# Kernel optimization log

Measured on AMD Instinct MI355X. Metric: run time of the kernel, lower is better.

## Reference

```python
import jax, jax.numpy as jnp
import numpy as np

D_MODEL = 2048
NUM_HEADS = 32
NUM_KV_HEADS = 8
D_K = D_MODEL // NUM_HEADS
B, S = 2, 2048


def setup_inputs() -> dict:
    key = jax.random.key(0)
    ks = jax.random.split(key, 6)
    sc = 1.0 / np.sqrt(D_MODEL)
    x = jax.random.normal(ks[0], (B, S, D_MODEL), dtype=jnp.float32)
    mask = jnp.tril(jnp.ones((S, S), dtype=jnp.float32))[None, None]  # [1,1,S,S]
    return {
        'x': x,
        'mask': mask,
        'Wq': jax.random.normal(ks[1], (D_MODEL, D_MODEL), jnp.float32) * sc,
        'bq': jnp.zeros((D_MODEL,), jnp.float32),
        'Wk': jax.random.normal(ks[2], (D_MODEL, NUM_KV_HEADS * D_K), jnp.float32) * sc,
        'bk': jnp.zeros((NUM_KV_HEADS * D_K,), jnp.float32),
        'Wv': jax.random.normal(ks[3], (D_MODEL, NUM_KV_HEADS * D_K), jnp.float32) * sc,
        'bv': jnp.zeros((NUM_KV_HEADS * D_K,), jnp.float32),
        'Wo': jax.random.normal(ks[4], (D_MODEL, D_MODEL), jnp.float32) * sc,
        'bo': jnp.zeros((D_MODEL,), jnp.float32),
    }


def reference(x, mask, Wq, bq, Wk, bk, Wv, bv, Wo, bo):
    b, s, _ = x.shape
    g = NUM_HEADS // NUM_KV_HEADS  # queries per kv head
    Q = (x @ Wq + bq).reshape(b, s, NUM_HEADS, D_K).transpose(0, 2, 1, 3)      # [b,h,s,dk]
    K = (x @ Wk + bk).reshape(b, s, NUM_KV_HEADS, D_K).transpose(0, 2, 1, 3)   # [b,kv,s,dk]
    V = (x @ Wv + bv).reshape(b, s, NUM_KV_HEADS, D_K).transpose(0, 2, 1, 3)
    # group queries per kv head instead of repeat_interleave on K/V
    Qg = Q.reshape(b, NUM_KV_HEADS, g, s, D_K)
    scores = jnp.einsum('bkgqd,bkld->bkgql', Qg, K) / np.sqrt(D_K)             # [b,kv,g,s,s]
    scores = jnp.where(mask[:, :, None] == 0, -1e9, scores)
    attn = jax.nn.softmax(scores, axis=-1)
    out = jnp.einsum('bkgql,bkld->bkgqd', attn, V)                              # [b,kv,g,s,dk]
    out = out.reshape(b, NUM_HEADS, s, D_K).transpose(0, 2, 1, 3).reshape(b, s, D_MODEL)
    return out @ Wo + bo
```

## Files before the change

### kernel.cpp

```cpp
#include <hip/hip_runtime.h>
#include <stdint.h>

typedef __bf16 bf16x8 __attribute__((ext_vector_type(8)));
typedef float  f32x4  __attribute__((ext_vector_type(4)));

__device__ __forceinline__ f32x4 mfma16(bf16x8 a, bf16x8 b, f32x4 c) {
    return __builtin_amdgcn_mfma_f32_16x16x32_bf16(a, b, c, 0, 0, 0);
}

__device__ __forceinline__ uint16_t f2bf(float f) {
    union { __bf16 b; uint16_t u; } cv; cv.b = (__bf16)f; return cv.u;
}

typedef __attribute__((address_space(3))) void as3_void;
typedef __attribute__((address_space(1))) void as1_void;
__device__ __forceinline__ void async_ld16(const void* g, void* l) {
    __builtin_amdgcn_global_load_lds((const as1_void*)g, (as3_void*)l, 16, 0, 0);
}


__global__ void convert_f32_bf16(const float* __restrict__ in, uint16_t* __restrict__ out, int n) {
    int i = (blockIdx.x * 256 + threadIdx.x) * 4;
    if (i >= n) return;
    float4 v = *(const float4*)(in + i);
    ushort4 o;
    o.x = f2bf(v.x); o.y = f2bf(v.y); o.z = f2bf(v.z); o.w = f2bf(v.w);
    *(ushort4*)(out + i) = o;
}

__global__ void transpose_f32_bf16(const float* __restrict__ in, uint16_t* __restrict__ out,
                                   int ldin, int out_off, int ldout) {
    __shared__ float tile[32][33];
    const int c0 = blockIdx.x << 5, r0 = blockIdx.y << 5;
    const int tx = threadIdx.x, ty = threadIdx.y;
#pragma unroll
    for (int i = 0; i < 4; ++i)
        tile[ty + i * 8][tx] = in[(size_t)(r0 + ty + i * 8) * ldin + c0 + tx];
    __syncthreads();
#pragma unroll
    for (int i = 0; i < 4; ++i)
        out[(size_t)(out_off + c0 + ty + i * 8) * ldout + r0 + tx] = f2bf(tile[tx][ty + i * 8]);
}

__global__ void transpose_v(const uint16_t* __restrict__ qkv, uint16_t* __restrict__ vt) {
    __shared__ uint16_t tile[32][33];
    const int c0 = blockIdx.x << 5, r0 = blockIdx.y << 5, b = blockIdx.z;
    const int tx = threadIdx.x, ty = threadIdx.y;
#pragma unroll
    for (int i = 0; i < 4; ++i)
        tile[ty + i * 8][tx] = qkv[(size_t)(b * 2048 + r0 + ty + i * 8) * 3072 + 2560 + c0 + tx];
    __syncthreads();
#pragma unroll
    for (int i = 0; i < 4; ++i)
        vt[(size_t)(b * 512 + c0 + ty + i * 8) * 2048 + r0 + tx] = tile[tx][ty + i * 8];
}

__global__ void concat_bias(const float* __restrict__ bq, const float* __restrict__ bk,
                            const float* __restrict__ bv, float* __restrict__ out) {
    int i = blockIdx.x * 256 + threadIdx.x;
    if (i >= 3072) return;
    out[i] = (i < 2048) ? bq[i] : (i < 2560 ? bk[i - 2048] : bv[i - 2560]);
}

template <bool F32OUT>
__global__ __launch_bounds__(256, 2)
void gemm_bt(const uint16_t* __restrict__ A, const uint16_t* __restrict__ Bt,
             const float* __restrict__ bias, void* __restrict__ Cout, int N, int K) {
    __shared__ __align__(16) uint16_t As[4096];
    __shared__ __align__(16) uint16_t Bs[4096];
    const int tid = threadIdx.x;
    const int wv = tid >> 6, ln = tid & 63;
    const int quad = ln >> 4, l16 = ln & 15;
    const int row0 = blockIdx.y << 7, col0 = blockIdx.x << 7;
    const int wm = wv >> 1, wn = wv & 1;

    const int p0 = tid, p1 = tid + 256;
    const int ar0 = p0 >> 2, ac0 = (p0 & 3) ^ ((ar0 ^ (ar0 >> 2)) & 3);
    const int ar1 = p1 >> 2, ac1 = (p1 & 3) ^ ((ar1 ^ (ar1 >> 2)) & 3);
    const uint16_t* gA0 = A + (size_t)(row0 + ar0) * K + (ac0 << 3);
    const uint16_t* gA1 = A + (size_t)(row0 + ar1) * K + (ac1 << 3);
    const uint16_t* gB0 = Bt + (size_t)(col0 + ar0) * K + (ac0 << 3);
    const uint16_t* gB1 = Bt + (size_t)(col0 + ar1) * K + (ac1 << 3);
    uint16_t* lA0 = As + (wv << 9);
    uint16_t* lA1 = As + 2048 + (wv << 9);
    uint16_t* lB0 = Bs + (wv << 9);
    uint16_t* lB1 = Bs + 2048 + (wv << 9);

    int a_off[4], b_off[4];
#pragma unroll
    for (int t = 0; t < 4; ++t) {
        int r = (wm << 6) + (t << 4) + l16;
        a_off[t] = (((r << 2) + (quad ^ ((r ^ (r >> 2)) & 3))) << 3);
        r = (wn << 6) + (t << 4) + l16;
        b_off[t] = (((r << 2) + (quad ^ ((r ^ (r >> 2)) & 3))) << 3);
    }

    f32x4 acc[4][4] = {};

    for (int k0 = 0; k0 < K; k0 += 32) {
        __syncthreads();
        async_ld16(gA0 + k0, lA0);
        async_ld16(gA1 + k0, lA1);
        async_ld16(gB0 + k0, lB0);
        async_ld16(gB1 + k0, lB1);
        __syncthreads();
        bf16x8 af[4], bfr[4];
#pragma unroll
        for (int t = 0; t < 4; ++t) af[t] = *(const bf16x8*)(As + a_off[t]);
#pragma unroll
        for (int t = 0; t < 4; ++t) bfr[t] = *(const bf16x8*)(Bs + b_off[t]);
#pragma unroll
        for (int mt = 0; mt < 4; ++mt)
#pragma unroll
            for (int nt = 0; nt < 4; ++nt)
                acc[mt][nt] = mfma16(af[mt], bfr[nt], acc[mt][nt]);
    }

#pragma unroll
    for (int nt = 0; nt < 4; ++nt) {
        const int col = col0 + (wn << 6) + (nt << 4) + l16;
        const float bv = bias[col];
#pragma unroll
        for (int mt = 0; mt < 4; ++mt) {
            const int rbase = row0 + (wm << 6) + (mt << 4) + (quad << 2);
#pragma unroll
            for (int r = 0; r < 4; ++r) {
                float v = acc[mt][nt][r] + bv;
                if (F32OUT)
                    ((float*)Cout)[(size_t)(rbase + r) * N + col] = v;
                else
                    ((uint16_t*)Cout)[(size_t)(rbase + r) * N + col] = f2bf(v);
            }
        }
    }
}

__global__ __launch_bounds__(256, 4)
void attn_fwd(const uint16_t* __restrict__ QKV, const uint16_t* __restrict__ Vt,
              uint16_t* __restrict__ AO) {
    __shared__ __align__(16) uint16_t Ks[2][2048];
    __shared__ __align__(16) uint16_t Vs[2][2048];
    __shared__ __align__(16) uint16_t Ps[4][640];

    const int tid = threadIdx.x;
    const int wv = tid >> 6, ln = tid & 63;
    const int quad = ln >> 4, l16 = ln & 15;
    const int p = blockIdx.x, kvh = blockIdx.y, b = blockIdx.z;
    const int h = kvh * 4 + wv;

    const uint16_t* Kg = QKV + (size_t)(b * 2048) * 3072 + 2048 + kvh * 64;
    const uint16_t* Vg = Vt + (size_t)(b * 512 + kvh * 64) * 2048;

    const int kr = tid >> 3, kc = (tid & 7) ^ (kr & 7);
    const int vr = tid >> 2, vc = (tid & 3) ^ ((vr ^ (vr >> 2)) & 3);
    const uint16_t* KgT = Kg + (size_t)kr * 3072 + kc * 8;
    const uint16_t* VgT = Vg + (size_t)vr * 2048 + vc * 8;

    int kf_off[2][2], vf_off[4];
#pragma unroll
    for (int nt = 0; nt < 2; ++nt)
#pragma unroll
        for (int kk = 0; kk < 2; ++kk) {
            int r = nt * 16 + l16, c = kk * 4 + quad;
            kf_off[nt][kk] = ((r << 3) + (c ^ (r & 7))) << 3;
        }
#pragma unroll
    for (int nt = 0; nt < 4; ++nt) {
        int r = nt * 16 + l16;
        vf_off[nt] = ((r << 2) + (quad ^ ((r ^ (r >> 2)) & 3))) << 3;
    }

#pragma unroll
    for (int half = 0; half < 2; ++half) {
        const int w = half ? (127 - p) : p;
        const int q0 = w << 4;

        bf16x8 qf[2];
#pragma unroll
        for (int kk = 0; kk < 2; ++kk)
            qf[kk] = *(const bf16x8*)(QKV +
                (size_t)(b * 2048 + q0 + l16) * 3072 + h * 64 + kk * 32 + quad * 8);

        f32x4 acc[4] = {};
        float lpart[4] = {};

        const int nkb = (w >> 1) + 1;
        __syncthreads();
        async_ld16(KgT, Ks[0] + (wv << 9));
        async_ld16(VgT, Vs[0] + (wv << 9));

        for (int kb = 0; kb < nkb; ++kb) {
            const int cur = kb & 1;
            const int key0 = kb << 5;
            __syncthreads();
            if (kb + 1 < nkb) {
                async_ld16(KgT + (size_t)((kb + 1) << 5) * 3072, Ks[cur ^ 1] + (wv << 9));
                async_ld16(VgT + ((kb + 1) << 5), Vs[cur ^ 1] + (wv << 9));
            }

            bf16x8 kf[2][2];
#pragma unroll
            for (int nt = 0; nt < 2; ++nt)
#pragma unroll
                for (int kk = 0; kk < 2; ++kk)
                    kf[nt][kk] = *(const bf16x8*)(Ks[cur] + kf_off[nt][kk]);
            bf16x8 vf[4];
#pragma unroll
            for (int nt = 0; nt < 4; ++nt)
                vf[nt] = *(const bf16x8*)(Vs[cur] + vf_off[nt]);

            f32x4 s0 = {0.f, 0.f, 0.f, 0.f}, s1 = {0.f, 0.f, 0.f, 0.f};
            s0 = mfma16(qf[0], kf[0][0], s0);
            s0 = mfma16(qf[1], kf[0][1], s0);
            s1 = mfma16(qf[0], kf[1][0], s1);
            s1 = mfma16(qf[1], kf[1][1], s1);

            const bool diag = (kb == nkb - 1);
#pragma unroll
            for (int r = 0; r < 4; ++r) {
                float e0 = __expf(fmaf(s0[r], 0.125f, -16.0f));
                float e1 = __expf(fmaf(s1[r], 0.125f, -16.0f));
                if (diag) {
                    const int qrow = q0 + quad * 4 + r;
                    if (key0 + l16 > qrow) e0 = 0.0f;
                    if (key0 + 16 + l16 > qrow) e1 = 0.0f;
                }
                lpart[r] += e0 + e1;
                const int prow = quad * 4 + r;
                Ps[wv][prow * 40 + l16] = f2bf(e0);
                Ps[wv][prow * 40 + 16 + l16] = f2bf(e1);
            }
            bf16x8 pf = *(const bf16x8*)(&Ps[wv][l16 * 40 + quad * 8]);
#pragma unroll
            for (int nt = 0; nt < 4; ++nt)
                acc[nt] = mfma16(pf, vf[nt], acc[nt]);
        }

        float inv[4];
#pragma unroll
        for (int r = 0; r < 4; ++r) {
            float rs = lpart[r];
#pragma unroll
            for (int off = 1; off < 16; off <<= 1)
                rs += __shfl_xor(rs, off, 64);
            inv[r] = 1.0f / rs;
        }
#pragma unroll
        for (int nt = 0; nt < 4; ++nt)
#pragma unroll
            for (int r = 0; r < 4; ++r) {
                const int qrow = q0 + quad * 4 + r;
                AO[(size_t)(b * 2048 + qrow) * 2048 + h * 64 + nt * 16 + l16] =
                    f2bf(acc[nt][r] * inv[r]);
            }
    }
}


extern "C" void kernel_launch(void* const* d_in, const int* in_sizes, int n_in,
                              void* d_out, int out_size, void* d_ws, size_t ws_size,
                              hipStream_t stream) {
    (void)in_sizes; (void)n_in; (void)out_size; (void)ws_size;
    const float* x  = (const float*)d_in[0];
    const float* Wq = (const float*)d_in[2];
    const float* bq = (const float*)d_in[3];
    const float* Wk = (const float*)d_in[4];
    const float* bk = (const float*)d_in[5];
    const float* Wv = (const float*)d_in[6];
    const float* bv = (const float*)d_in[7];
    const float* Wo = (const float*)d_in[8];
    const float* bo = (const float*)d_in[9];

    char* ws = (char*)d_ws;
    uint16_t* xb    = (uint16_t*)ws;
    uint16_t* wqkvT = (uint16_t*)(ws + 16777216);
    uint16_t* woT   = (uint16_t*)(ws + 16777216 + 12582912);
    float*    biasq = (float*)(ws + 16777216 + 12582912 + 8388608);
    uint16_t* qkv   = (uint16_t*)d_out;
    uint16_t* ao    = xb;
    uint16_t* vt    = wqkvT;

    dim3 tb(32, 8);
    convert_f32_bf16<<<8192, 256, 0, stream>>>(x, xb, 4096 * 2048);
    transpose_f32_bf16<<<dim3(64, 64), tb, 0, stream>>>(Wq, wqkvT, 2048, 0,    2048);
    transpose_f32_bf16<<<dim3(16, 64), tb, 0, stream>>>(Wk, wqkvT, 512,  2048, 2048);
    transpose_f32_bf16<<<dim3(16, 64), tb, 0, stream>>>(Wv, wqkvT, 512,  2560, 2048);
    transpose_f32_bf16<<<dim3(64, 64), tb, 0, stream>>>(Wo, woT,   2048, 0,    2048);
    concat_bias<<<12, 256, 0, stream>>>(bq, bk, bv, biasq);

    gemm_bt<false><<<dim3(24, 32), 256, 0, stream>>>(xb, wqkvT, biasq, qkv, 3072, 2048);
    transpose_v<<<dim3(16, 64, 2), tb, 0, stream>>>(qkv, vt);
    attn_fwd<<<dim3(64, 8, 2), 256, 0, stream>>>(qkv, vt, ao);
    gemm_bt<true><<<dim3(16, 32), 256, 0, stream>>>(ao, woT, bo, d_out, 2048, 2048);
}
```

Before: 329.6 us.

## Transpose attention MFMA operands to keep P in registers and triple-buffer K/V

The attention kernel now computes S^T (K as the A operand), so the exponentiated probabilities of each lane form a bf16x8 B operand directly. This removes the per-block LDS round trip through Ps. V^T is written with a column permutation so the key order matches the new P register layout. K/V staging moves to three buffers, and the QK^T for the next block is issued while the current block's softmax and PV run. The diagonal mask is peeled out of the loop. Output is staged through LDS for 16-byte coalesced stores. The cost is more LDS and register pressure, which could reduce occupancy.

Result: no change. 323.4 us (-1.9%).

```diff
diff --git a/kernel.cpp b/kernel.cpp
--- a/kernel.cpp
+++ b/kernel.cpp
@@ -50,9 +50,10 @@
     for (int i = 0; i < 4; ++i)
         tile[ty + i * 8][tx] = qkv[(size_t)(b * 2048 + r0 + ty + i * 8) * 3072 + 2560 + c0 + tx];
     __syncthreads();
+    const int perm = 4 * (tx >> 3) + (((tx & 7) < 4) ? 0 : 16) + (tx & 3);
 #pragma unroll
     for (int i = 0; i < 4; ++i)
-        vt[(size_t)(b * 512 + c0 + ty + i * 8) * 2048 + r0 + tx] = tile[tx][ty + i * 8];
+        vt[(size_t)(b * 512 + c0 + ty + i * 8) * 2048 + r0 + tx] = tile[perm][ty + i * 8];
 }
 
 __global__ void concat_bias(const float* __restrict__ bq, const float* __restrict__ bk,
@@ -138,9 +139,9 @@
 __global__ __launch_bounds__(256, 4)
 void attn_fwd(const uint16_t* __restrict__ QKV, const uint16_t* __restrict__ Vt,
               uint16_t* __restrict__ AO) {
-    __shared__ __align__(16) uint16_t Ks[2][2048];
-    __shared__ __align__(16) uint16_t Vs[2][2048];
-    __shared__ __align__(16) uint16_t Ps[4][640];
+    __shared__ __align__(16) uint16_t Ks[3][2048];
+    __shared__ __align__(16) uint16_t Vs[3][2048];
+    __shared__ __align__(16) uint16_t Ot[4][1088];
 
     const int tid = threadIdx.x;
     const int wv = tid >> 6, ln = tid & 63;
@@ -155,6 +156,7 @@
     const int vr = tid >> 2, vc = (tid & 3) ^ ((vr ^ (vr >> 2)) & 3);
     const uint16_t* KgT = Kg + (size_t)kr * 3072 + kc * 8;
     const uint16_t* VgT = Vg + (size_t)vr * 2048 + vc * 8;
+    const int sdst = wv << 9;
 
     int kf_off[2][2], vf_off[4];
 #pragma unroll
@@ -174,6 +176,7 @@
     for (int half = 0; half < 2; ++half) {
         const int w = half ? (127 - p) : p;
         const int q0 = w << 4;
+        const int nkb = (w >> 1) + 1;
 
         bf16x8 qf[2];
 #pragma unroll
@@ -182,77 +185,113 @@
                 (size_t)(b * 2048 + q0 + l16) * 3072 + h * 64 + kk * 32 + quad * 8);
 
         f32x4 acc[4] = {};
-        float lpart[4] = {};
-
-        const int nkb = (w >> 1) + 1;
+        float lp = 0.0f;
+
         __syncthreads();
-        async_ld16(KgT, Ks[0] + (wv << 9));
-        async_ld16(VgT, Vs[0] + (wv << 9));
-
-        for (int kb = 0; kb < nkb; ++kb) {
-            const int cur = kb & 1;
-            const int key0 = kb << 5;
+        async_ld16(KgT, Ks[0] + sdst);
+        async_ld16(VgT, Vs[0] + sdst);
+        __syncthreads();
+        if (nkb > 1) {
+            async_ld16(KgT + (size_t)32 * 3072, Ks[1] + sdst);
+            async_ld16(VgT + 32, Vs[1] + sdst);
+        }
+
+        f32x4 s0 = {0.f, 0.f, 0.f, 0.f}, s1 = {0.f, 0.f, 0.f, 0.f};
+        {
+            bf16x8 k00 = *(const bf16x8*)(Ks[0] + kf_off[0][0]);
+            bf16x8 k01 = *(const bf16x8*)(Ks[0] + kf_off[0][1]);
+            bf16x8 k10 = *(const bf16x8*)(Ks[0] + kf_off[1][0]);
+            bf16x8 k11 = *(const bf16x8*)(Ks[0] + kf_off[1][1]);
+            s0 = mfma16(k00, qf[0], s0); s0 = mfma16(k01, qf[1], s0);
+            s1 = mfma16(k10, qf[0], s1); s1 = mfma16(k11, qf[1], s1);
+        }
+
+        int cur = 0, nxt = 1, pf2 = 2;
+        for (int t = 0; t < nkb - 1; ++t) {
             __syncthreads();
-            if (kb + 1 < nkb) {
-                async_ld16(KgT + (size_t)((kb + 1) << 5) * 3072, Ks[cur ^ 1] + (wv << 9));
-                async_ld16(VgT + ((kb + 1) << 5), Vs[cur ^ 1] + (wv << 9));
+            if (t + 2 < nkb) {
+                async_ld16(KgT + (size_t)((t + 2) << 5) * 3072, Ks[pf2] + sdst);
+                async_ld16(VgT + ((t + 2) << 5), Vs[pf2] + sdst);
             }
-
-            bf16x8 kf[2][2];
-#pragma unroll
-            for (int nt = 0; nt < 2; ++nt)
-#pragma unroll
-                for (int kk = 0; kk < 2; ++kk)
-                    kf[nt][kk] = *(const bf16x8*)(Ks[cur] + kf_off[nt][kk]);
             bf16x8 vf[4];
 #pragma unroll
             for (int nt = 0; nt < 4; ++nt)
                 vf[nt] = *(const bf16x8*)(Vs[cur] + vf_off[nt]);
-
-            f32x4 s0 = {0.f, 0.f, 0.f, 0.f}, s1 = {0.f, 0.f, 0.f, 0.f};
-            s0 = mfma16(qf[0], kf[0][0], s0);
-            s0 = mfma16(qf[1], kf[0][1], s0);
-            s1 = mfma16(qf[0], kf[1][0], s1);
-            s1 = mfma16(qf[1], kf[1][1], s1);
-
-            const bool diag = (kb == nkb - 1);
+            bf16x8 k00 = *(const bf16x8*)(Ks[nxt] + kf_off[0][0]);
+            bf16x8 k01 = *(const bf16x8*)(Ks[nxt] + kf_off[0][1]);
+            bf16x8 k10 = *(const bf16x8*)(Ks[nxt] + kf_off[1][0]);
+            bf16x8 k11 = *(const bf16x8*)(Ks[nxt] + kf_off[1][1]);
+
+            float e0 = __expf(fmaf(s0[0], 0.125f, -16.0f));
+            float e1 = __expf(fmaf(s0[1], 0.125f, -16.0f));
+            float e2 = __expf(fmaf(s0[2], 0.125f, -16.0f));
+            float e3 = __expf(fmaf(s0[3], 0.125f, -16.0f));
+            float e4 = __expf(fmaf(s1[0], 0.125f, -16.0f));
+            float e5 = __expf(fmaf(s1[1], 0.125f, -16.0f));
+            float e6 = __expf(fmaf(s1[2], 0.125f, -16.0f));
+            float e7 = __expf(fmaf(s1[3], 0.125f, -16.0f));
+            lp += ((e0 + e1) + (e2 + e3)) + ((e4 + e5) + (e6 + e7));
+            bf16x8 pf;
+            pf[0] = (__bf16)e0; pf[1] = (__bf16)e1; pf[2] = (__bf16)e2; pf[3] = (__bf16)e3;
+            pf[4] = (__bf16)e4; pf[5] = (__bf16)e5; pf[6] = (__bf16)e6; pf[7] = (__bf16)e7;
+
+            f32x4 n0 = {0.f, 0.f, 0.f, 0.f}, n1 = {0.f, 0.f, 0.f, 0.f};
+            n0 = mfma16(k00, qf[0], n0); n0 = mfma16(k01, qf[1], n0);
+            n1 = mfma16(k10, qf[0], n1); n1 = mfma16(k11, qf[1], n1);
+
+#pragma unroll
+            for (int nt = 0; nt < 4; ++nt)
+                acc[nt] = mfma16(vf[nt], pf, acc[nt]);
+
+            s0 = n0; s1 = n1;
+            int o = cur; cur = nxt; nxt = pf2; pf2 = o;
+        }
+
+        {
+            const int key0 = (nkb - 1) << 5;
+            bf16x8 vf[4];
+#pragma unroll
+            for (int nt = 0; nt < 4; ++nt)
+                vf[nt] = *(const bf16x8*)(Vs[cur] + vf_off[nt]);
+            const int qrow = q0 + l16;
+            float e[8];
 #pragma unroll
             for (int r = 0; r < 4; ++r) {
-                float e0 = __expf(fmaf(s0[r], 0.125f, -16.0f));
-                float e1 = __expf(fmaf(s1[r], 0.125f, -16.0f));
-                if (diag) {
-                    const int qrow = q0 + quad * 4 + r;
-                    if (key0 + l16 > qrow) e0 = 0.0f;
-                    if (key0 + 16 + l16 > qrow) e1 = 0.0f;
-                }
-                lpart[r] += e0 + e1;
-                const int prow = quad * 4 + r;
-                Ps[wv][prow * 40 + l16] = f2bf(e0);
-                Ps[wv][prow * 40 + 16 + l16] = f2bf(e1);
+                float v0 = __expf(fmaf(s0[r], 0.125f, -16.0f));
+                float v1 = __expf(fmaf(s1[r], 0.125f, -16.0f));
+                if (key0 + quad * 4 + r > qrow) v0 = 0.0f;
+                if (key0 + 16 + quad * 4 + r > qrow) v1 = 0.0f;
+                e[r] = v0; e[4 + r] = v1;
             }
-            bf16x8 pf = *(const bf16x8*)(&Ps[wv][l16 * 40 + quad * 8]);
-#pragma unroll
-            for (int nt = 0; nt < 4; ++nt)
-                acc[nt] = mfma16(pf, vf[nt], acc[nt]);
-        }
-
-        float inv[4];
-#pragma unroll
-        for (int r = 0; r < 4; ++r) {
-            float rs = lpart[r];
-#pragma unroll
-            for (int off = 1; off < 16; off <<= 1)
-                rs += __shfl_xor(rs, off, 64);
-            inv[r] = 1.0f / rs;
-        }
+            lp += ((e[0] + e[1]) + (e[2] + e[3])) + ((e[4] + e[5]) + (e[6] + e[7]));
+            bf16x8 pf;
+#pragma unroll
+            for (int j = 0; j < 8; ++j) pf[j] = (__bf16)e[j];
+#pragma unroll
+            for (int nt = 0; nt < 4; ++nt)
+                acc[nt] = mfma16(vf[nt], pf, acc[nt]);
+        }
+
+        float rs = lp;
+        rs += __shfl_xor(rs, 16, 64);
+        rs += __shfl_xor(rs, 32, 64);
+        const float inv = 1.0f / rs;
+
+        uint16_t* ot = Ot[wv];
 #pragma unroll
         for (int nt = 0; nt < 4; ++nt)
 #pragma unroll
-            for (int r = 0; r < 4; ++r) {
-                const int qrow = q0 + quad * 4 + r;
-                AO[(size_t)(b * 2048 + qrow) * 2048 + h * 64 + nt * 16 + l16] =
-                    f2bf(acc[nt][r] * inv[r]);
+            for (int pp = 0; pp < 2; ++pp) {
+                uint32_t pk = (uint32_t)f2bf(acc[nt][2 * pp] * inv) |
+                              ((uint32_t)f2bf(acc[nt][2 * pp + 1] * inv) << 16);
+                *(uint32_t*)(ot + l16 * 68 + nt * 16 + quad * 4 + 2 * pp) = pk;
             }
+        const int orow = ln >> 2, oc = ln & 3;
+        uint4 o1 = *(const uint4*)(ot + orow * 68 + oc * 8);
+        uint4 o2 = *(const uint4*)(ot + orow * 68 + (4 + oc) * 8);
+        uint16_t* aobase = AO + (size_t)(b * 2048 + q0 + orow) * 2048 + h * 64;
+        *(uint4*)(aobase + oc * 8) = o1;
+        *(uint4*)(aobase + (4 + oc) * 8) = o2;
     }
 }
 
```
